# Kernel optimization log

Hardware: AMD Instinct MI355X
Metric: run time of the kernel (lower is better)

The kernel has to match this reference:

```python
import jax, jax.numpy as jnp
import numpy as np

D_MODEL = 1024
N_HEADS = 16
D_HEAD = D_MODEL // N_HEADS
B, T = 4, 2048


def layernorm(x, g, b, eps=1e-5):
    mu = jnp.mean(x, axis=-1, keepdims=True)
    var = jnp.mean((x - mu) ** 2, axis=-1, keepdims=True)
    return (x - mu) * jax.lax.rsqrt(var + eps) * g + b


def setup_inputs() -> dict:
    key = jax.random.key(0)
    ks = jax.random.split(key, 12)
    s_in = 1.0 / np.sqrt(D_MODEL)
    s_ff = 1.0 / np.sqrt(4 * D_MODEL)
    return {
        "x": jax.random.normal(ks[0], (B, T, D_MODEL), jnp.float32),
        "Wq": jax.random.normal(ks[1], (N_HEADS, D_MODEL, D_HEAD), jnp.float32) * s_in,
        "Wk": jax.random.normal(ks[2], (N_HEADS, D_MODEL, D_HEAD), jnp.float32) * s_in,
        "Wv": jax.random.normal(ks[3], (N_HEADS, D_MODEL, D_HEAD), jnp.float32) * s_in,
        "Wproj": jax.random.normal(ks[4], (D_MODEL, D_MODEL), jnp.float32) * s_in,
        "bproj": jnp.zeros((D_MODEL,), jnp.float32),
        "W1": jax.random.normal(ks[5], (D_MODEL, 4 * D_MODEL), jnp.float32) * s_in,
        "b1": jnp.zeros((4 * D_MODEL,), jnp.float32),
        "W2": jax.random.normal(ks[6], (4 * D_MODEL, D_MODEL), jnp.float32) * s_ff,
        "b2": jnp.zeros((D_MODEL,), jnp.float32),
        "g1": jnp.ones((D_MODEL,), jnp.float32),
        "beta1": jnp.zeros((D_MODEL,), jnp.float32),
        "g2": jnp.ones((D_MODEL,), jnp.float32),
        "beta2": jnp.zeros((D_MODEL,), jnp.float32),
    }


def reference(x, Wq, Wk, Wv, Wproj, bproj, W1, b1, W2, b2, g1, beta1, g2, beta2):
    Bb, Tt, C = x.shape
    # x = ln1(x); residual uses the NORMALIZED x (quirk of original module)
    x1 = layernorm(x, g1, beta1)
    # all heads at once: [B,H,T,Dh]
    q = jnp.einsum("btd,hdk->bhtk", x1, Wq)
    k = jnp.einsum("btd,hdk->bhtk", x1, Wk)
    v = jnp.einsum("btd,hdk->bhtk", x1, Wv)
    # NOTE: original scales by 1/sqrt(C) with C = d_model, not d_head
    wei = jnp.einsum("bhtk,bhsk->bhts", q, k) / np.sqrt(C).astype(np.float32)
    causal = jnp.tril(jnp.ones((Tt, Tt), bool))
    wei = jnp.where(causal, wei, -jnp.inf)
    wei = jax.nn.softmax(wei, axis=-1)
    attn = jnp.einsum("bhts,bhsk->bhtk", wei, v)  # [B,H,T,Dh]
    attn = attn.transpose(0, 2, 1, 3).reshape(Bb, Tt, C)  # concat heads
    sa = attn @ Wproj + bproj
    x2 = x1 + sa
    # x = ln2(x); residual again uses the normalized tensor
    x3 = layernorm(x2, g2, beta2)
    h = jax.nn.relu(x3 @ W1 + b1)
    ff = h @ W2 + b2
    return x3 + ff
```

## Files before the change

kernel.cpp:

```cpp
#include <hip/hip_runtime.h>
#include <cstdint>

typedef _Float16 f16;
typedef __attribute__((ext_vector_type(8))) _Float16 f16x8;
typedef __attribute__((ext_vector_type(4))) _Float16 f16x4;
typedef __attribute__((ext_vector_type(2))) _Float16 f16x2;
typedef __attribute__((ext_vector_type(4))) float f32x4;
typedef __attribute__((ext_vector_type(16))) float f32x16;

#define D_MODEL 1024
#define T_SEQ   2048
#define NTOK    8192
#define DFF     4096
#define DHEAD   64

struct alignas(16) H8 { f16 h[8]; };

__device__ __forceinline__ void load_lds16(const void* gp, void* lp) {
  __builtin_amdgcn_global_load_lds(
      (const __attribute__((address_space(1))) unsigned int*)(unsigned long long)(uintptr_t)gp,
      (__attribute__((address_space(3))) unsigned int*)(unsigned int)(uintptr_t)lp,
      16, 0, 0);
}

__global__ __launch_bounds__(256) void transpose_pack(
    const float* __restrict__ in, f16* __restrict__ out,
    int rows, int cols, long long in_slice, long long out_slice)
{
  __shared__ float tile[32][33];
  const float* inp = in + (size_t)blockIdx.z * in_slice;
  f16* outp = out + (size_t)blockIdx.z * out_slice;
  int r0 = blockIdx.x * 32, c0 = blockIdx.y * 32;
  int tx = threadIdx.x & 31, ty = threadIdx.x >> 5;
  #pragma unroll
  for (int i = 0; i < 4; ++i)
    tile[ty + i*8][tx] = inp[(size_t)(r0 + ty + i*8)*cols + c0 + tx];
  __syncthreads();
  #pragma unroll
  for (int i = 0; i < 4; ++i)
    outp[(size_t)(c0 + ty + i*8)*rows + r0 + tx] = (f16)tile[tx][ty + i*8];
}

__global__ __launch_bounds__(256) void ln_kernel(
    const float* __restrict__ x, const float* __restrict__ g, const float* __restrict__ b,
    float* __restrict__ outf, f16* __restrict__ outh)
{
  int row = blockIdx.x;
  const float* xr = x + (size_t)row * D_MODEL;
  int tid = threadIdx.x;
  float v[4];
  float s = 0.f;
  #pragma unroll
  for (int i = 0; i < 4; ++i) { v[i] = xr[tid + i*256]; s += v[i]; }
  #pragma unroll
  for (int off = 32; off > 0; off >>= 1) s += __shfl_down(s, off, 64);
  __shared__ float red1[4], red2[4];
  if ((tid & 63) == 0) red1[tid >> 6] = s;
  __syncthreads();
  float mean = (red1[0] + red1[1] + red1[2] + red1[3]) * (1.f / D_MODEL);
  float s2 = 0.f;
  #pragma unroll
  for (int i = 0; i < 4; ++i) { float d = v[i] - mean; s2 += d * d; }
  #pragma unroll
  for (int off = 32; off > 0; off >>= 1) s2 += __shfl_down(s2, off, 64);
  if ((tid & 63) == 0) red2[tid >> 6] = s2;
  __syncthreads();
  float var = (red2[0] + red2[1] + red2[2] + red2[3]) * (1.f / D_MODEL);
  float rstd = rsqrtf(var + 1e-5f);
  #pragma unroll
  for (int i = 0; i < 4; ++i) {
    int c = tid + i*256;
    float y = (v[i] - mean) * rstd * g[c] + b[c];
    outf[(size_t)row*D_MODEL + c] = y;
    outh[(size_t)row*D_MODEL + c] = (f16)y;
  }
}

template<int MODE>
__global__ __launch_bounds__(256) void gemm_kernel(
    const f16* __restrict__ A, const f16* __restrict__ BT, int K,
    const float* __restrict__ bias, const float* __restrict__ resid,
    float* __restrict__ outf, f16* __restrict__ o0, f16* __restrict__ o1, f16* __restrict__ o2)
{
  constexpr int BM = 128, BN = 128, BK = 64;
  __shared__ __align__(16) f16 As[BM * BK];
  __shared__ __align__(16) f16 Bs[BN * BK];
  int tid  = threadIdx.x;
  int lane = tid & 63;
  int wave = tid >> 6;
  int wm = (wave >> 1) * 64, wn = (wave & 1) * 64;
  size_t row0 = (size_t)blockIdx.x * BM, col0 = (size_t)blockIdx.y * BN;
  int rl = lane & 31;
  int half = lane >> 5;
  int swz = rl & 7;

  f32x16 acc[2][2];
  #pragma unroll
  for (int i = 0; i < 2; ++i)
    #pragma unroll
    for (int j = 0; j < 2; ++j)
      acc[i][j] = (f32x16)(0.f);

  const f16* a_base = A  + row0 * K;
  const f16* b_base = BT + col0 * K;

  for (int k0 = 0; k0 < K; k0 += BK) {
    __syncthreads();
    #pragma unroll
    for (int i = 0; i < 4; ++i) {
      int c  = tid + i * 256;
      int rr = c >> 3;
      int cg = (c & 7) ^ (rr & 7);
      load_lds16(a_base + (size_t)rr * K + k0 + cg * 8, As + (size_t)(c & ~63) * 8);
      load_lds16(b_base + (size_t)rr * K + k0 + cg * 8, Bs + (size_t)(c & ~63) * 8);
    }
    __syncthreads();
    #pragma unroll
    for (int ks = 0; ks < 4; ++ks) {
      int chunk = (ks * 2 + half) ^ swz;
      f16x8 fa[2], fb[2];
      #pragma unroll
      for (int mi = 0; mi < 2; ++mi)
        fa[mi] = *(const f16x8*)(As + (wm + mi*32 + rl) * BK + chunk * 8);
      #pragma unroll
      for (int ni = 0; ni < 2; ++ni)
        fb[ni] = *(const f16x8*)(Bs + (wn + ni*32 + rl) * BK + chunk * 8);
      #pragma unroll
      for (int mi = 0; mi < 2; ++mi)
        #pragma unroll
        for (int ni = 0; ni < 2; ++ni)
          acc[mi][ni] = __builtin_amdgcn_mfma_f32_32x32x16_f16(fa[mi], fb[ni], acc[mi][ni], 0, 0, 0);
    }
  }

  int rbase = half * 4;
  #pragma unroll
  for (int mi = 0; mi < 2; ++mi) {
    #pragma unroll
    for (int ni = 0; ni < 2; ++ni) {
      #pragma unroll
      for (int r = 0; r < 16; ++r) {
        size_t grow = row0 + wm + mi*32 + rbase + (r & 3) + 8 * (r >> 2);
        size_t gcol = col0 + wn + ni*32 + rl;
        float v = acc[mi][ni][r];
        if constexpr (MODE == 0) {
          int sel = (int)(gcol >> 10);
          int hh  = ((int)gcol >> 6) & 15;
          int dd  = (int)gcol & 63;
          f16* dst = (sel == 0) ? o0 : ((sel == 1) ? o1 : o2);
          if (sel == 0) v *= 0.045084229f;
          size_t bh = (grow >> 11) * 16 + hh;
          dst[(bh * T_SEQ + (grow & 2047)) * DHEAD + dd] = (f16)v;
        } else if constexpr (MODE == 1 || MODE == 3) {
          size_t idx = grow * D_MODEL + gcol;
          outf[idx] = v + bias[gcol] + resid[idx];
        } else {
          float t = v + bias[gcol];
          o0[grow * (size_t)DFF + gcol] = (f16)(t > 0.f ? t : 0.f);
        }
      }
    }
  }
}

__global__ __launch_bounds__(256) void attn_mfma(
    const f16* __restrict__ qb, const f16* __restrict__ kb,
    const f16* __restrict__ vb, f16* __restrict__ attnb)
{
  constexpr int KT  = 64;
  constexpr int LDK = 72;
  __shared__ __align__(16) f16 Kl[KT * LDK];
  __shared__ __align__(16) f16 Vt[DHEAD * LDK];
  __shared__ __align__(16) f16 Pt[4 * 32 * LDK];

  int tid  = threadIdx.x;
  int lane = tid & 63, wave = tid >> 6;
  int n    = lane & 15, quad = lane >> 4;
  int quad4 = quad * 4;
  int bh   = blockIdx.y;

  const f16* qg = qb + (size_t)bh * T_SEQ * DHEAD;
  const f16* kg = kb + (size_t)bh * T_SEQ * DHEAD;
  const f16* vg = vb + (size_t)bh * T_SEQ * DHEAD;
  f16* Ptw = Pt + wave * 32 * LDK;
  size_t orow = (size_t)(bh >> 4) * T_SEQ;
  int hcol = (bh & 15) * DHEAD;

  #pragma unroll
  for (int pass = 0; pass < 2; ++pass) {
    int qi = pass == 0 ? (15 - (int)blockIdx.x) : (int)blockIdx.x;
    int qw = qi * 128 + wave * 32;

    f16x8 qfrag[2][2];
    #pragma unroll
    for (int ni = 0; ni < 2; ++ni)
      #pragma unroll
      for (int kj = 0; kj < 2; ++kj)
        qfrag[ni][kj] = *(const f16x8*)(qg + (size_t)(qw + ni*16 + n)*DHEAD + kj*32 + quad*8);

    f32x4 o[2][4];
    #pragma unroll
    for (int mb = 0; mb < 2; ++mb)
      #pragma unroll
      for (int di = 0; di < 4; ++di) o[mb][di] = f32x4{0.f,0.f,0.f,0.f};
    float lsum[2] = {0.f, 0.f};

    int ntiles = 2 * qi + 2;
    for (int kt = 0; kt < ntiles; ++kt) {
      int kt0 = kt * KT;
      __syncthreads();
      #pragma unroll
      for (int it = 0; it < 2; ++it) {
        int idx = tid + it * 256;
        int key = idx >> 3, dq = idx & 7;
        *(uint4*)(Kl + key * LDK + dq * 8) =
            *(const uint4*)(kg + (size_t)(kt0 + key) * DHEAD + dq * 8);
      }
      {
        int kp = tid & 31, dblk = tid >> 5;
        const f16* v0 = vg + (size_t)(kt0 + 2*kp) * DHEAD + dblk * 8;
        H8 va = *(const H8*)v0;
        H8 vbv = *(const H8*)(v0 + DHEAD);
        #pragma unroll
        for (int e = 0; e < 8; ++e) {
          f16x2 pk2; pk2[0] = va.h[e]; pk2[1] = vbv.h[e];
          *(f16x2*)(Vt + (dblk*8 + e) * LDK + 2*kp) = pk2;
        }
      }
      __syncthreads();

      if (kt0 > qw + 31) continue;
      bool need_mask = (kt0 + KT - 1) > qw;

      f32x4 st[4][2];
      #pragma unroll
      for (int mi = 0; mi < 4; ++mi)
        #pragma unroll
        for (int ni = 0; ni < 2; ++ni) st[mi][ni] = f32x4{0.f,0.f,0.f,0.f};
      #pragma unroll
      for (int kj = 0; kj < 2; ++kj) {
        #pragma unroll
        for (int mi = 0; mi < 4; ++mi) {
          f16x8 kf = *(const f16x8*)(Kl + (mi*16 + n) * LDK + kj*32 + quad*8);
          #pragma unroll
          for (int ni = 0; ni < 2; ++ni)
            st[mi][ni] = __builtin_amdgcn_mfma_f32_16x16x32_f16(kf, qfrag[ni][kj], st[mi][ni], 0, 0, 0);
        }
      }

      #pragma unroll
      for (int ni = 0; ni < 2; ++ni) {
        #pragma unroll
        for (int mi = 0; mi < 4; ++mi) {
          f16x4 pk;
          #pragma unroll
          for (int r = 0; r < 4; ++r) {
            float sv = st[mi][ni][r];
            if (need_mask) {
              int key = kt0 + mi*16 + quad4 + r;
              int qq  = qw  + ni*16 + n;
              if (key > qq) sv = -1e30f;
            }
            float p = __builtin_amdgcn_exp2f(sv);
            lsum[ni] += p;
            pk[r] = (f16)p;
          }
          *(f16x4*)(Ptw + (ni*16 + n) * LDK + mi*16 + quad4) = pk;
        }
      }

      #pragma unroll
      for (int kj = 0; kj < 2; ++kj) {
        f16x8 pf[2];
        #pragma unroll
        for (int mb = 0; mb < 2; ++mb)
          pf[mb] = *(const f16x8*)(Ptw + (mb*16 + n) * LDK + kj*32 + quad*8);
        #pragma unroll
        for (int di = 0; di < 4; ++di) {
          f16x8 vf = *(const f16x8*)(Vt + (di*16 + n) * LDK + kj*32 + quad*8);
          #pragma unroll
          for (int mb = 0; mb < 2; ++mb)
            o[mb][di] = __builtin_amdgcn_mfma_f32_16x16x32_f16(pf[mb], vf, o[mb][di], 0, 0, 0);
        }
      }
    }

    #pragma unroll
    for (int ni = 0; ni < 2; ++ni) {
      lsum[ni] += __shfl_xor(lsum[ni], 16, 64);
      lsum[ni] += __shfl_xor(lsum[ni], 32, 64);
    }
    #pragma unroll
    for (int mb = 0; mb < 2; ++mb) {
      #pragma unroll
      for (int r = 0; r < 4; ++r) {
        float lv  = __shfl(lsum[mb], quad4 + r, 64);
        float inv = 1.f / lv;
        int t = qw + mb*16 + quad4 + r;
        #pragma unroll
        for (int di = 0; di < 4; ++di)
          attnb[(orow + t) * D_MODEL + hcol + di*16 + n] = (f16)(o[mb][di][r] * inv);
      }
    }
  }
}

extern "C" void kernel_launch(void* const* d_in, const int* in_sizes, int n_in,
                              void* d_out, int out_size, void* d_ws, size_t ws_size,
                              hipStream_t stream)
{
  const float* x     = (const float*)d_in[0];
  const float* Wq    = (const float*)d_in[1];
  const float* Wk    = (const float*)d_in[2];
  const float* Wv    = (const float*)d_in[3];
  const float* Wproj = (const float*)d_in[4];
  const float* bproj = (const float*)d_in[5];
  const float* W1    = (const float*)d_in[6];
  const float* b1    = (const float*)d_in[7];
  const float* W2    = (const float*)d_in[8];
  const float* b2    = (const float*)d_in[9];
  const float* g1    = (const float*)d_in[10];
  const float* bt1   = (const float*)d_in[11];
  const float* g2    = (const float*)d_in[12];
  const float* bt2   = (const float*)d_in[13];
  float* out = (float*)d_out;
  (void)in_sizes; (void)n_in; (void)out_size; (void)ws_size;

  char* ws = (char*)d_ws;
  const size_t SZ_H16 = (size_t)NTOK * D_MODEL * 2;
  const size_t SZ_F32 = (size_t)NTOK * D_MODEL * 4;
  f16*   qb      = (f16*)(ws + 0);
  f16*   kb      = (f16*)(ws + 1 * SZ_H16);
  f16*   vb      = (f16*)(ws + 2 * SZ_H16);
  f16*   attnb   = (f16*)(ws + 3 * SZ_H16);
  f16*   hbuf    = (f16*)(ws + 0);
  float* x1f     = (float*)(ws + 4 * SZ_H16);
  f16*   x1h     = (f16*)(ws + 4 * SZ_H16 + SZ_F32);
  float* x3f     = (float*)(ws + 5 * SZ_H16 + SZ_F32);
  f16*   x3h     = (f16*)(ws + 5 * SZ_H16 + 2 * SZ_F32);
  char*  wb      = ws + 6 * SZ_H16 + 2 * SZ_F32;
  f16*   Wqkv_t  = (f16*)(wb);
  f16*   Wproj_t = (f16*)(wb + (size_t)3072*1024*2);
  f16*   W1_t    = (f16*)(wb + (size_t)(3072+1024)*1024*2);
  f16*   W2_t    = (f16*)(wb + (size_t)(3072+1024+4096)*1024*2);

  dim3 blk(256);
  transpose_pack<<<dim3(32, 2, 16), blk, 0, stream>>>(Wq, Wqkv_t,                 1024, 64,  65536, 65536);
  transpose_pack<<<dim3(32, 2, 16), blk, 0, stream>>>(Wk, Wqkv_t + 1024*1024,     1024, 64,  65536, 65536);
  transpose_pack<<<dim3(32, 2, 16), blk, 0, stream>>>(Wv, Wqkv_t + 2*1024*1024,   1024, 64,  65536, 65536);
  transpose_pack<<<dim3(32, 32, 1), blk, 0, stream>>>(Wproj, Wproj_t, 1024, 1024, 0, 0);
  transpose_pack<<<dim3(32, 128, 1), blk, 0, stream>>>(W1, W1_t, 1024, 4096, 0, 0);
  transpose_pack<<<dim3(128, 32, 1), blk, 0, stream>>>(W2, W2_t, 4096, 1024, 0, 0);
  ln_kernel<<<NTOK, blk, 0, stream>>>(x, g1, bt1, x1f, x1h);
  gemm_kernel<0><<<dim3(64, 24), blk, 0, stream>>>(x1h, Wqkv_t, 1024, nullptr, nullptr, nullptr, qb, kb, vb);
  attn_mfma<<<dim3(8, 64), blk, 0, stream>>>(qb, kb, vb, attnb);
  gemm_kernel<1><<<dim3(64, 8), blk, 0, stream>>>(attnb, Wproj_t, 1024, bproj, x1f, x1f, nullptr, nullptr, nullptr);
  ln_kernel<<<NTOK, blk, 0, stream>>>(x1f, g2, bt2, x3f, x3h);
  gemm_kernel<2><<<dim3(64, 32), blk, 0, stream>>>(x3h, W1_t, 1024, b1, nullptr, nullptr, hbuf, nullptr, nullptr);
  gemm_kernel<3><<<dim3(64, 8), blk, 0, stream>>>(hbuf, W2_t, 4096, b2, x3f, out, nullptr, nullptr, nullptr);
}
```

Baseline: 529.6 us.

## Replace GEMM with 512-thread double-buffered pipelined kernel using larger tiles

Rewrites the GEMM as an 8-wave kernel with 256-row tiles (256x256 for the FFN up-projection). It double-buffers LDS and interleaves async global-to-LDS staging with MFMA phases separated by explicit barriers and vmcnt waits. It also adds an XCD-aware block remap and raises MFMA priority with setprio. The aim is to hide global load latency and raise data reuse per tile. The cost is more LDS and register pressure, and fewer workgroups, which can hurt occupancy and tail balance on the smaller projection GEMMs.

```diff
diff --git a/kernel.cpp b/kernel.cpp
--- a/kernel.cpp
+++ b/kernel.cpp
@@ -21,6 +21,23 @@
       (const __attribute__((address_space(1))) unsigned int*)(unsigned long long)(uintptr_t)gp,
       (__attribute__((address_space(3))) unsigned int*)(unsigned int)(uintptr_t)lp,
       16, 0, 0);
+}
+
+__device__ __forceinline__ void phase_bar() {
+  asm volatile("" ::: "memory");
+  __builtin_amdgcn_sched_barrier(0);
+  __builtin_amdgcn_s_barrier();
+  __builtin_amdgcn_sched_barrier(0);
+  asm volatile("" ::: "memory");
+}
+
+__device__ __forceinline__ void wait_vm2() {
+  asm volatile("s_waitcnt vmcnt(2)" ::: "memory");
+  __builtin_amdgcn_sched_barrier(0);
+}
+__device__ __forceinline__ void wait_vm0() {
+  asm volatile("s_waitcnt vmcnt(0)" ::: "memory");
+  __builtin_amdgcn_sched_barrier(0);
 }
 
 __global__ __launch_bounds__(256) void transpose_pack(
@@ -76,71 +93,162 @@
   }
 }
 
-template<int MODE>
-__global__ __launch_bounds__(256) void gemm_kernel(
+
+#define STAGE_H(gbase, h, ldst, k0)                                            \
+  { _Pragma("unroll")                                                          \
+    for (int j_ = 0; j_ < 2; ++j_) {                                           \
+      int c_  = tid + j_*512;                                                  \
+      int rr_ = c_ >> 3;                                                       \
+      int cg_ = (c_ & 7) ^ (rr_ & 7);                                          \
+      load_lds16((gbase) + (size_t)((h)*128 + rr_) * K + (k0) + cg_*8,         \
+                 (ldst) + (h)*128*64 + (size_t)(c_ & ~63) * 8);                \
+    } }
+
+#define LDS_A(bsel, mp)                                                        \
+  { _Pragma("unroll")                                                          \
+    for (int i_ = 0; i_ < 2; ++i_)                                             \
+      _Pragma("unroll")                                                        \
+      for (int ks_ = 0; ks_ < 4; ++ks_)                                        \
+        fa[i_][ks_] = *(const f16x8*)(&As[bsel][                               \
+            (wm + ((mp)*2 + i_)*32 + rl)*64 + (((ks_*2 + hl) ^ sw)*8)]); }
+
+#define LDS_B(bsel, ni, fb)                                                    \
+  { _Pragma("unroll")                                                          \
+    for (int ks_ = 0; ks_ < 4; ++ks_)                                          \
+      fb[ks_] = *(const f16x8*)(&Bs[bsel][                                     \
+          (wn + (ni)*32 + rl)*64 + (((ks_*2 + hl) ^ sw)*8)]); }
+
+#define MFMA8(mp, ni, fb)                                                      \
+  { __builtin_amdgcn_s_setprio(1);                                             \
+    _Pragma("unroll")                                                          \
+    for (int ks_ = 0; ks_ < 4; ++ks_) {                                        \
+      acc[(mp)*2+0][ni] = __builtin_amdgcn_mfma_f32_32x32x16_f16(              \
+          fa[0][ks_], fb[ks_], acc[(mp)*2+0][ni], 0, 0, 0);                    \
+      acc[(mp)*2+1][ni] = __builtin_amdgcn_mfma_f32_32x32x16_f16(              \
+          fa[1][ks_], fb[ks_], acc[(mp)*2+1][ni], 0, 0, 0);                    \
+    }                                                                          \
+    __builtin_amdgcn_s_setprio(0); }
+
+template<int MODE, int BN>
+__global__ __launch_bounds__(512, 2) void gemm8(
     const f16* __restrict__ A, const f16* __restrict__ BT, int K,
     const float* __restrict__ bias, const float* __restrict__ resid,
     float* __restrict__ outf, f16* __restrict__ o0, f16* __restrict__ o1, f16* __restrict__ o2)
 {
-  constexpr int BM = 128, BN = 128, BK = 64;
-  __shared__ __align__(16) f16 As[BM * BK];
-  __shared__ __align__(16) f16 Bs[BN * BK];
+  constexpr int BM  = 256;
+  constexpr int NWN = BN / 64;
+  constexpr int MI  = (BM / (8 / NWN)) / 32;
+
+  __shared__ __align__(16) f16 As[2][BM * 64];
+  __shared__ __align__(16) f16 Bs[2][BN * 64];
+
   int tid  = threadIdx.x;
   int lane = tid & 63;
   int wave = tid >> 6;
-  int wm = (wave >> 1) * 64, wn = (wave & 1) * 64;
-  size_t row0 = (size_t)blockIdx.x * BM, col0 = (size_t)blockIdx.y * BN;
-  int rl = lane & 31;
-  int half = lane >> 5;
-  int swz = rl & 7;
-
-  f32x16 acc[2][2];
-  #pragma unroll
-  for (int i = 0; i < 2; ++i)
+  int rl = lane & 31, hl = lane >> 5;
+  int sw = rl & 7;
+  int wmi = wave / NWN, wni = wave % NWN;
+  int wm = wmi * (MI * 32), wn = wni * 64;
+
+  int gx  = gridDim.x;
+  int nwg = gx * gridDim.y;
+  int lin = blockIdx.x + gx * blockIdx.y;
+  int sid = (nwg & 7) == 0 ? ((lin & 7) * (nwg >> 3) + (lin >> 3)) : lin;
+  int bx  = sid % gx, by = sid / gx;
+
+  size_t row0 = (size_t)bx * BM, col0 = (size_t)by * BN;
+  const f16* a_base = A  + row0 * K;
+  const f16* b_base = BT + col0 * K;
+  int NT = K >> 6;
+
+  f32x16 acc[MI][2];
+  #pragma unroll
+  for (int i = 0; i < MI; ++i)
     #pragma unroll
     for (int j = 0; j < 2; ++j)
       acc[i][j] = (f32x16)(0.f);
 
-  const f16* a_base = A  + row0 * K;
-  const f16* b_base = BT + col0 * K;
-
-  for (int k0 = 0; k0 < K; k0 += BK) {
-    __syncthreads();
-    #pragma unroll
-    for (int i = 0; i < 4; ++i) {
-      int c  = tid + i * 256;
-      int rr = c >> 3;
-      int cg = (c & 7) ^ (rr & 7);
-      load_lds16(a_base + (size_t)rr * K + k0 + cg * 8, As + (size_t)(c & ~63) * 8);
-      load_lds16(b_base + (size_t)rr * K + k0 + cg * 8, Bs + (size_t)(c & ~63) * 8);
-    }
-    __syncthreads();
-    #pragma unroll
-    for (int ks = 0; ks < 4; ++ks) {
-      int chunk = (ks * 2 + half) ^ swz;
-      f16x8 fa[2], fb[2];
-      #pragma unroll
-      for (int mi = 0; mi < 2; ++mi)
-        fa[mi] = *(const f16x8*)(As + (wm + mi*32 + rl) * BK + chunk * 8);
-      #pragma unroll
-      for (int ni = 0; ni < 2; ++ni)
-        fb[ni] = *(const f16x8*)(Bs + (wn + ni*32 + rl) * BK + chunk * 8);
-      #pragma unroll
-      for (int mi = 0; mi < 2; ++mi)
-        #pragma unroll
-        for (int ni = 0; ni < 2; ++ni)
-          acc[mi][ni] = __builtin_amdgcn_mfma_f32_32x32x16_f16(fa[mi], fb[ni], acc[mi][ni], 0, 0, 0);
+  f16x8 fa[2][4], fb0[4], fb1[4];
+
+  if constexpr (BN == 256) {
+    STAGE_H(a_base, 0, &As[0][0], 0);
+    STAGE_H(a_base, 1, &As[0][0], 0);
+    STAGE_H(b_base, 0, &Bs[0][0], 0);
+    STAGE_H(b_base, 1, &Bs[0][0], 0);
+    if (NT > 1) { STAGE_H(a_base, 0, &As[1][0], 64); wait_vm2(); }
+    else        { wait_vm0(); }
+    phase_bar();
+
+    for (int t = 0; t < NT; ++t) {
+      int cur = t & 1, nxt = cur ^ 1;
+      int k1 = (t + 1) << 6, k2 = (t + 2) << 6;
+      bool s1 = (t + 1) < NT, s2 = (t + 2) < NT;
+      LDS_A(cur, 0); LDS_B(cur, 0, fb0);
+      if (s1) STAGE_H(a_base, 1, &As[nxt][0], k1);
+      phase_bar();
+      MFMA8(0, 0, fb0);
+      phase_bar();
+      LDS_B(cur, 1, fb1);
+      if (s1) STAGE_H(b_base, 0, &Bs[nxt][0], k1);
+      phase_bar();
+      MFMA8(0, 1, fb1);
+      phase_bar();
+      LDS_A(cur, 1);
+      if (s1) STAGE_H(b_base, 1, &Bs[nxt][0], k1);
+      phase_bar();
+      MFMA8(1, 0, fb0);
+      phase_bar();
+      if (s2) STAGE_H(a_base, 0, &As[cur][0], k2);
+      phase_bar();
+      MFMA8(1, 1, fb1);
+      if (s2) wait_vm2(); else wait_vm0();
+      phase_bar();
+    }
+  } else {
+    STAGE_H(a_base, 0, &As[0][0], 0);
+    STAGE_H(a_base, 1, &As[0][0], 0);
+    STAGE_H(b_base, 0, &Bs[0][0], 0);
+    if (NT > 1) { STAGE_H(a_base, 0, &As[1][0], 64); wait_vm2(); }
+    else        { wait_vm0(); }
+    phase_bar();
+
+    for (int t = 0; t < NT; t += 2) {
+      int k1 = (t + 1) << 6, k2 = (t + 2) << 6, k3 = (t + 3) << 6;
+      bool s1 = (t + 1) < NT, s2 = (t + 2) < NT, s3 = (t + 3) < NT;
+      LDS_A(0, 0); LDS_B(0, 0, fb0);
+      if (s1) { STAGE_H(a_base, 1, &As[1][0], k1); STAGE_H(b_base, 0, &Bs[1][0], k1); }
+      phase_bar();
+      MFMA8(0, 0, fb0);
+      phase_bar();
+      LDS_B(0, 1, fb1);
+      if (s2) STAGE_H(a_base, 0, &As[0][0], k2);
+      phase_bar();
+      MFMA8(0, 1, fb1);
+      if (s2) wait_vm2(); else wait_vm0();
+      phase_bar();
+      if (!s1) break;
+      LDS_A(1, 0); LDS_B(1, 0, fb0);
+      if (s2) { STAGE_H(a_base, 1, &As[0][0], k2); STAGE_H(b_base, 0, &Bs[0][0], k2); }
+      phase_bar();
+      MFMA8(0, 0, fb0);
+      phase_bar();
+      LDS_B(1, 1, fb1);
+      if (s3) STAGE_H(a_base, 0, &As[1][0], k3);
+      phase_bar();
+      MFMA8(0, 1, fb1);
+      if (s3) wait_vm2(); else wait_vm0();
+      phase_bar();
     }
   }
 
-  int rbase = half * 4;
-  #pragma unroll
-  for (int mi = 0; mi < 2; ++mi) {
+  int rb = hl * 4;
+  #pragma unroll
+  for (int mi = 0; mi < MI; ++mi) {
     #pragma unroll
     for (int ni = 0; ni < 2; ++ni) {
       #pragma unroll
       for (int r = 0; r < 16; ++r) {
-        size_t grow = row0 + wm + mi*32 + rbase + (r & 3) + 8 * (r >> 2);
+        size_t grow = row0 + wm + mi*32 + rb + (r & 3) + 8 * (r >> 2);
         size_t gcol = col0 + wn + ni*32 + rl;
         float v = acc[mi][ni][r];
         if constexpr (MODE == 0) {
@@ -344,7 +452,7 @@
   f16*   W1_t    = (f16*)(wb + (size_t)(3072+1024)*1024*2);
   f16*   W2_t    = (f16*)(wb + (size_t)(3072+1024+4096)*1024*2);
 
-  dim3 blk(256);
+  dim3 blk(256), blk5(512);
   transpose_pack<<<dim3(32, 2, 16), blk, 0, stream>>>(Wq, Wqkv_t,                 1024, 64,  65536, 65536);
   transpose_pack<<<dim3(32, 2, 16), blk, 0, stream>>>(Wk, Wqkv_t + 1024*1024,     1024, 64,  65536, 65536);
   transpose_pack<<<dim3(32, 2, 16), blk, 0, stream>>>(Wv, Wqkv_t + 2*1024*1024,   1024, 64,  65536, 65536);
@@ -352,10 +460,10 @@
   transpose_pack<<<dim3(32, 128, 1), blk, 0, stream>>>(W1, W1_t, 1024, 4096, 0, 0);
   transpose_pack<<<dim3(128, 32, 1), blk, 0, stream>>>(W2, W2_t, 4096, 1024, 0, 0);
   ln_kernel<<<NTOK, blk, 0, stream>>>(x, g1, bt1, x1f, x1h);
-  gemm_kernel<0><<<dim3(64, 24), blk, 0, stream>>>(x1h, Wqkv_t, 1024, nullptr, nullptr, nullptr, qb, kb, vb);
+  gemm8<0,128><<<dim3(32, 24), blk5, 0, stream>>>(x1h, Wqkv_t, 1024, nullptr, nullptr, nullptr, qb, kb, vb);
   attn_mfma<<<dim3(8, 64), blk, 0, stream>>>(qb, kb, vb, attnb);
-  gemm_kernel<1><<<dim3(64, 8), blk, 0, stream>>>(attnb, Wproj_t, 1024, bproj, x1f, x1f, nullptr, nullptr, nullptr);
+  gemm8<1,128><<<dim3(32, 8), blk5, 0, stream>>>(attnb, Wproj_t, 1024, bproj, x1f, x1f, nullptr, nullptr, nullptr);
   ln_kernel<<<NTOK, blk, 0, stream>>>(x1f, g2, bt2, x3f, x3h);
-  gemm_kernel<2><<<dim3(64, 32), blk, 0, stream>>>(x3h, W1_t, 1024, b1, nullptr, nullptr, hbuf, nullptr, nullptr);
-  gemm_kernel<3><<<dim3(64, 8), blk, 0, stream>>>(hbuf, W2_t, 4096, b2, x3f, out, nullptr, nullptr, nullptr);
-}
+  gemm8<2,256><<<dim3(32, 16), blk5, 0, stream>>>(x3h, W1_t, 1024, b1, nullptr, nullptr, hbuf, nullptr, nullptr);
+  gemm8<3,128><<<dim3(32, 8), blk5, 0, stream>>>(hbuf, W2_t, 4096, b2, x3f, out, nullptr, nullptr, nullptr);
+}
```

Result: faster. 519.1 us (-2.0%).
